# Performance work log

Hardware: AMD Instinct MI355X
Metric: run time of the kernel (lower is better)

The kernel has to match this reference:

```python
import jax, jax.numpy as jnp
import numpy as np

N_NODES = 100000
E = 1600000
IN_C = 128
OUT_C = 128


def setup_inputs() -> dict:
    key = jax.random.key(0)
    k1, k2, k3, k4, k5, k6 = jax.random.split(key, 6)
    x = jax.random.normal(k1, (N_NODES, IN_C), dtype=jnp.float32)
    edge_index = jax.random.randint(k2, (2, E), 0, N_NODES, dtype=jnp.int64)
    s = 1.0 / np.sqrt(IN_C)
    W_src = jax.random.uniform(k3, (OUT_C, IN_C), minval=-s, maxval=s, dtype=jnp.float32)
    b_src = jax.random.uniform(k4, (OUT_C,), minval=-s, maxval=s, dtype=jnp.float32)
    W_dst = jax.random.uniform(k5, (OUT_C, IN_C), minval=-s, maxval=s, dtype=jnp.float32)
    b_dst = jax.random.uniform(k6, (OUT_C,), minval=-s, maxval=s, dtype=jnp.float32)
    return {"x": x, "edge_index": edge_index, "W_src": W_src, "b_src": b_src,
            "W_dst": W_dst, "b_dst": b_dst}


def reference(x, edge_index, W_src, b_src, W_dst, b_dst):
    src, dst = edge_index[0], edge_index[1]
    x_j = x[src]                                             # [E, in]
    agg_sum = jax.ops.segment_sum(x_j, dst, num_segments=x.shape[0])   # [N, in]
    cnt = jax.ops.segment_sum(jnp.ones((src.shape[0],), dtype=x.dtype), dst,
                              num_segments=x.shape[0])       # [N]
    agg_mean = agg_sum / jnp.maximum(cnt, 1.0)[:, None]      # scatter-mean (empty -> 0)
    return agg_mean @ W_src.T + b_src + x @ W_dst.T + b_dst
```

## Files before the change

### kernel.cpp

```cpp
#include <hip/hip_runtime.h>
#include <stdint.h>

typedef __attribute__((ext_vector_type(8))) short short8;
typedef __attribute__((ext_vector_type(4))) float floatx4;
typedef __attribute__((ext_vector_type(4))) int intx4;
typedef __attribute__((ext_vector_type(2))) int intx2;
typedef __attribute__((ext_vector_type(2))) float floatx2;

#define NN 100000
#define NE 1600000
#define NB_SCAN 196
#define HIST_BLKS 6250
#define CONV_BLKS 6250
#define NODES_PER_G 12500
#define CAP 64

#define NBKT 196
#define TILE 4096
#define BIN_BLKS 391
#define CAPB 8704

__device__ __forceinline__ short f2bf(float f) {
  unsigned u = __builtin_bit_cast(unsigned, f);
  u = (u + 0x7fffu + ((u >> 16) & 1u)) >> 16;
  return (short)u;
}
__device__ __forceinline__ float bf2f(unsigned hi16) {
  return __builtin_bit_cast(float, hi16 << 16);
}

#define BK_GC_B 0
#define BK_GBUF_B 4096
#define BK_SLOT_B 14000000
#define BK_ROW_B 21000000
#define BK_DEG_B 21500000
#define BK_XB_B 22000000
#define BK_XQ_B 47600000
#define BK_NEED 60400000ull

#define WS_DEG 0
#define WS_ROW 100000
#define WS_CUR 200000
#define WS_BSUM 300000
#define WS_BOFF 300256
#define WS_SLOT 300512
#define WS_XB_BYTE 7602048


__global__ __launch_bounds__(256) void bin_conv_k(const int* __restrict__ ei,
                                                  int* __restrict__ gcount,
                                                  int2* __restrict__ gbuf,
                                                  const float* __restrict__ x,
                                                  short* __restrict__ xb,
                                                  int* __restrict__ xq) {
  const int blk = blockIdx.x;
  if (blk < BIN_BLKS) {
    __shared__ int ls[TILE], ld[TILE];
    __shared__ int hcnt[NBKT], hbase[NBKT], hcur[NBKT], gposs[NBKT];
    __shared__ int sc[256];
    __shared__ int ntot;
    const int tid = threadIdx.x;
    const int tile = blk * TILE;

    int s_[16], d_[16];
#pragma unroll
    for (int k = 0; k < 16; ++k) {
      const int e = tile + tid + k * 256;
      if (e < NE) {
        s_[k] = ei[e];
        d_[k] = ei[NE + e];
      } else {
        s_[k] = 0; d_[k] = -1;
      }
    }
    if (tid < NBKT) hcnt[tid] = 0;
    __syncthreads();
#pragma unroll
    for (int k = 0; k < 16; ++k)
      if (d_[k] >= 0) atomicAdd(&hcnt[d_[k] >> 9], 1);
    __syncthreads();
    sc[tid] = (tid < NBKT) ? hcnt[tid] : 0;
    __syncthreads();
    for (int off = 1; off < 256; off <<= 1) {
      const int v = (tid >= off) ? sc[tid - off] : 0;
      __syncthreads();
      sc[tid] += v;
      __syncthreads();
    }
    if (tid < NBKT) {
      hbase[tid] = sc[tid] - hcnt[tid];
      gposs[tid] = atomicAdd(&gcount[tid], hcnt[tid]);
      hcur[tid] = 0;
    }
    if (tid == 0) ntot = sc[NBKT - 1];
    __syncthreads();
#pragma unroll
    for (int k = 0; k < 16; ++k) {
      if (d_[k] >= 0) {
        const int b = d_[k] >> 9;
        const int r = hbase[b] + atomicAdd(&hcur[b], 1);
        ls[r] = s_[k];
        ld[r] = d_[k];
      }
    }
    __syncthreads();
    const int nt = ntot;
    for (int i = tid; i < nt; i += 256) {
      const int d = ld[i];
      const int b = d >> 9;
      const int pos = gposs[b] + (i - hbase[b]);
      if (pos < CAPB) {
        int2 e; e.x = ls[i]; e.y = d;
        gbuf[(size_t)b * CAPB + pos] = e;
      }
    }
  } else {
    const int t = (blk - BIN_BLKS) * 256 + threadIdx.x;
    const floatx4* x4 = reinterpret_cast<const floatx4*>(x);
    floatx4 f0 = __builtin_nontemporal_load(&x4[2 * t]);
    floatx4 f1 = __builtin_nontemporal_load(&x4[2 * t + 1]);
    short8 v;
    v[0] = f2bf(f0.x); v[1] = f2bf(f0.y); v[2] = f2bf(f0.z); v[3] = f2bf(f0.w);
    v[4] = f2bf(f1.x); v[5] = f2bf(f1.y); v[6] = f2bf(f1.z); v[7] = f2bf(f1.w);
    reinterpret_cast<short8*>(xb)[t] = v;
    int w0 = __builtin_amdgcn_cvt_pk_fp8_f32(f0.x, f0.y, 0, false);
    w0 = __builtin_amdgcn_cvt_pk_fp8_f32(f0.z, f0.w, w0, true);
    int w1 = __builtin_amdgcn_cvt_pk_fp8_f32(f1.x, f1.y, 0, false);
    w1 = __builtin_amdgcn_cvt_pk_fp8_f32(f1.z, f1.w, w1, true);
    intx2 q; q.x = w0; q.y = w1;
    reinterpret_cast<intx2*>(xq)[t] = q;
  }
}

__global__ __launch_bounds__(512) void bucket_csr_k(const int* __restrict__ gcount,
                                                    const int2* __restrict__ gbuf,
                                                    int* __restrict__ slotg,
                                                    int* __restrict__ rowstg,
                                                    int* __restrict__ degg) {
  __shared__ int cnt[512], sc[512], cur[512];
  __shared__ int lslot[CAPB];
  const int b = blockIdx.x;
  const int tid = threadIdx.x;
  const int nb = min(gcount[b], CAPB);
  const size_t base = (size_t)b * CAPB;

  cnt[tid] = 0;
  __syncthreads();
  for (int i = tid; i < nb; i += 512)
    atomicAdd(&cnt[gbuf[base + i].y & 511], 1);
  __syncthreads();
  sc[tid] = cnt[tid];
  __syncthreads();
  for (int off = 1; off < 512; off <<= 1) {
    const int v = (tid >= off) ? sc[tid - off] : 0;
    __syncthreads();
    sc[tid] += v;
    __syncthreads();
  }
  const int rst = sc[tid] - cnt[tid];
  cur[tid] = rst;
  __syncthreads();
  for (int i = tid; i < nb; i += 512) {
    const int2 e = gbuf[base + i];
    const int p = atomicAdd(&cur[e.y & 511], 1);
    lslot[p] = e.x << 6;
  }
  __syncthreads();
  for (int i = tid; i < nb; i += 512) slotg[base + i] = lslot[i];
  const int n = b * 512 + tid;
  if (n < NN) {
    rowstg[n] = (int)base + rst;
    degg[n] = cnt[tid];
  }
}

__global__ __launch_bounds__(256) void gather_csr_k(const unsigned short* __restrict__ xq,
                                                    const int* __restrict__ rowstg,
                                                    const int* __restrict__ degg,
                                                    const int* __restrict__ slotg,
                                                    float* __restrict__ out) {
  const int lane = threadIdx.x & 63;
  const int w = (blockIdx.x * 256 + threadIdx.x) >> 6;
  if (w >= NN) return;
  const int st = rowstg[w];
  const int dg = degg[w];
  float2 acc = {0.f, 0.f};
  for (int b0 = 0; b0 < dg; b0 += 64) {
    const int nbk = min(64, dg - b0);
    const int idx = (lane < nbk) ? slotg[st + b0 + lane] : 0;
    int i = 0;
    for (; i + 4 <= nbk; i += 4) {
      const int s0 = __shfl(idx, i), s1 = __shfl(idx, i + 1);
      const int s2 = __shfl(idx, i + 2), s3 = __shfl(idx, i + 3);
      const int v0 = xq[s0 + lane];
      const int v1 = xq[s1 + lane];
      const int v2 = xq[s2 + lane];
      const int v3 = xq[s3 + lane];
      floatx2 p0 = __builtin_amdgcn_cvt_pk_f32_fp8(v0, false);
      floatx2 p1 = __builtin_amdgcn_cvt_pk_f32_fp8(v1, false);
      floatx2 p2 = __builtin_amdgcn_cvt_pk_f32_fp8(v2, false);
      floatx2 p3 = __builtin_amdgcn_cvt_pk_f32_fp8(v3, false);
      acc.x += p0.x; acc.y += p0.y;
      acc.x += p1.x; acc.y += p1.y;
      acc.x += p2.x; acc.y += p2.y;
      acc.x += p3.x; acc.y += p3.y;
    }
    for (; i < nbk; ++i) {
      const int s = __shfl(idx, i);
      const int v = xq[s + lane];
      floatx2 p = __builtin_amdgcn_cvt_pk_f32_fp8(v, false);
      acc.x += p.x; acc.y += p.y;
    }
  }
  const float inv = 1.0f / fmaxf((float)dg, 1.0f);
  const unsigned b0w = (unsigned)(unsigned short)f2bf(acc.x * inv);
  const unsigned b1w = (unsigned)(unsigned short)f2bf(acc.y * inv);
  reinterpret_cast<unsigned*>(out + (size_t)w * 128 + 64)[lane] = b0w | (b1w << 16);
}


__global__ __launch_bounds__(256) void hist_conv_k(const int* __restrict__ ei,
                                                   int* __restrict__ deg,
                                                   const float* __restrict__ x,
                                                   short* __restrict__ xb) {
  const int b = blockIdx.x;
  if (b < HIST_BLKS) {
    int e = b * 256 + threadIdx.x;
    if (e < NE) atomicAdd(&deg[ei[NE + e]], 1);
  } else {
    const int t = (b - HIST_BLKS) * 256 + threadIdx.x;
    const float4* x4 = reinterpret_cast<const float4*>(x);
    float4 f0 = x4[2 * t];
    float4 f1 = x4[2 * t + 1];
    short8 v;
    v[0] = f2bf(f0.x); v[1] = f2bf(f0.y); v[2] = f2bf(f0.z); v[3] = f2bf(f0.w);
    v[4] = f2bf(f1.x); v[5] = f2bf(f1.y); v[6] = f2bf(f1.z); v[7] = f2bf(f1.w);
    reinterpret_cast<short8*>(xb)[t] = v;
  }
}

__global__ __launch_bounds__(256) void scan1_k(const int* __restrict__ deg,
                                               int* __restrict__ bsum) {
  __shared__ int s[256];
  const int t = threadIdx.x;
  const int i0 = blockIdx.x * 512 + 2 * t;
  int v = 0;
  if (i0 < NN) v += deg[i0];
  if (i0 + 1 < NN) v += deg[i0 + 1];
  s[t] = v;
  __syncthreads();
  for (int off = 128; off > 0; off >>= 1) {
    if (t < off) s[t] += s[t + off];
    __syncthreads();
  }
  if (t == 0) bsum[blockIdx.x] = s[0];
}

__global__ __launch_bounds__(256) void scan2_k(const int* __restrict__ bsum,
                                               int* __restrict__ boff) {
  __shared__ int s[256];
  const int t = threadIdx.x;
  const int v = (t < NB_SCAN) ? bsum[t] : 0;
  s[t] = v;
  __syncthreads();
  for (int off = 1; off < 256; off <<= 1) {
    int a = (t >= off) ? s[t - off] : 0;
    __syncthreads();
    s[t] += a;
    __syncthreads();
  }
  if (t < NB_SCAN) boff[t] = s[t] - v;
}

__global__ __launch_bounds__(256) void scan3_k(const int* __restrict__ deg,
                                               const int* __restrict__ boff,
                                               int* __restrict__ rowst,
                                               int* __restrict__ cursor) {
  __shared__ int s[256];
  const int t = threadIdx.x;
  const int i0 = blockIdx.x * 512 + 2 * t;
  const int v0 = (i0 < NN) ? deg[i0] : 0;
  const int v1 = (i0 + 1 < NN) ? deg[i0 + 1] : 0;
  const int tsum = v0 + v1;
  s[t] = tsum;
  __syncthreads();
  for (int off = 1; off < 256; off <<= 1) {
    int a = (t >= off) ? s[t - off] : 0;
    __syncthreads();
    s[t] += a;
    __syncthreads();
  }
  const int excl = s[t] - tsum + boff[blockIdx.x];
  if (i0 < NN) { rowst[i0] = excl; cursor[i0] = excl; }
  if (i0 + 1 < NN) { rowst[i0 + 1] = excl + v0; cursor[i0 + 1] = excl + v0; }
}

__global__ __launch_bounds__(256) void fill_k(const int* __restrict__ ei,
                                              int* __restrict__ cursor,
                                              int* __restrict__ slot) {
  const int g = blockIdx.x & 7;
  const int lo = g * NODES_PER_G;
  const int hi = lo + NODES_PER_G;
  const int stride = (gridDim.x >> 3) * 256;
  for (int e = (blockIdx.x >> 3) * 256 + threadIdx.x; e < NE; e += stride) {
    const int d = ei[NE + e];
    if (d >= lo && d < hi) {
      const int p = atomicAdd(&cursor[d], 1);
      slot[p] = ei[e];
    }
  }
}

__global__ __launch_bounds__(256) void gather_bf_k(const short* __restrict__ xb,
                                                   const int* __restrict__ rowst,
                                                   const int* __restrict__ deg,
                                                   const int* __restrict__ slot,
                                                   float* __restrict__ out) {
  const int lane = threadIdx.x & 63;
  const int w = (blockIdx.x * 256 + threadIdx.x) >> 6;
  if (w >= NN) return;
  const int st = rowst[w];
  const int dg = deg[w];
  const unsigned* xu = reinterpret_cast<const unsigned*>(xb);
  float2 acc = {0.f, 0.f};
  for (int b0 = 0; b0 < dg; b0 += 64) {
    const int nb = min(64, dg - b0);
    const int idx = (lane < nb) ? slot[st + b0 + lane] : 0;
    for (int i = 0; i < nb; ++i) {
      const int s = __shfl(idx, i);
      unsigned u = xu[(size_t)s * 64 + lane];
      acc.x += bf2f(u & 0xffffu); acc.y += bf2f(u >> 16);
    }
  }
  const float inv = 1.0f / fmaxf((float)dg, 1.0f);
  const unsigned b0w = (unsigned)(unsigned short)f2bf(acc.x * inv);
  const unsigned b1w = (unsigned)(unsigned short)f2bf(acc.y * inv);
  reinterpret_cast<unsigned*>(out + (size_t)w * 128 + 64)[lane] = b0w | (b1w << 16);
}

__global__ __launch_bounds__(512) void sage_gemm_k(
    const short* __restrict__ xb,
    const float* __restrict__ Wsrc, const float* __restrict__ bsrc,
    const float* __restrict__ Wdst, const float* __restrict__ bdst,
    float* __restrict__ out) {
  __shared__ short Alds[128 * 128];
  __shared__ short Blds[128 * 128];
  const int tid = threadIdx.x;
  const int n0 = blockIdx.x * 128;

  const int wid = tid >> 6;
  const int lane = tid & 63;
  const int r0 = wid * 16;
  const int lrow = lane & 15;
  const int kh = (lane >> 4) * 8;
  const int arow = r0 + lrow;
  const int asw = (arow & 7) << 4;

  floatx4 acc[8];
  floatx4 zero = {0.f, 0.f, 0.f, 0.f};
#pragma unroll
  for (int f = 0; f < 8; ++f) acc[f] = zero;

#pragma unroll
  for (int h = 0; h < 2; ++h) {
    {
      const int j = tid >> 2;
      const int q = tid & 3;
      const float* src = ((h == 0) ? Wsrc : Wdst) + j * 128 + q * 32;
      const int sw = (j & 7) << 4;
      const int base = j * 256 + q * 64;
#pragma unroll
      for (int c = 0; c < 4; ++c) {
        float4 f0 = reinterpret_cast<const float4*>(src)[2 * c];
        float4 f1 = reinterpret_cast<const float4*>(src)[2 * c + 1];
        short8 v;
        v[0] = f2bf(f0.x); v[1] = f2bf(f0.y); v[2] = f2bf(f0.z); v[3] = f2bf(f0.w);
        v[4] = f2bf(f1.x); v[5] = f2bf(f1.y); v[6] = f2bf(f1.z); v[7] = f2bf(f1.w);
        *reinterpret_cast<short8*>(reinterpret_cast<char*>(Blds) + ((base + c * 16) ^ sw)) = v;
      }
    }
    {
      const int r = tid >> 2;
      const int q = tid & 3;
      const int n = n0 + r;
      const int sw = (r & 7) << 4;
      const int base = r * 256 + q * 64;
      if (n < NN) {
        const char* srcb = (h == 0)
            ? (reinterpret_cast<const char*>(out + (size_t)n * 128 + 64) + q * 64)
            : (reinterpret_cast<const char*>(xb + (size_t)n * 128) + q * 64);
#pragma unroll
        for (int c = 0; c < 4; ++c) {
          short8 v = *reinterpret_cast<const short8*>(srcb + c * 16);
          *reinterpret_cast<short8*>(reinterpret_cast<char*>(Alds) + ((base + c * 16) ^ sw)) = v;
        }
      } else {
        short8 z = {};
#pragma unroll
        for (int c = 0; c < 4; ++c)
          *reinterpret_cast<short8*>(reinterpret_cast<char*>(Alds) + ((base + c * 16) ^ sw)) = z;
      }
    }
    __syncthreads();

#pragma unroll
    for (int ks = 0; ks < 4; ++ks) {
      const int kb = (ks * 32 + kh) * 2;
      short8 a = *reinterpret_cast<const short8*>(
          reinterpret_cast<const char*>(Alds) + ((arow * 256 + kb) ^ asw));
#pragma unroll
      for (int f = 0; f < 8; ++f) {
        const int j = f * 16 + lrow;
        short8 b = *reinterpret_cast<const short8*>(
            reinterpret_cast<const char*>(Blds) + ((j * 256 + kb) ^ ((j & 7) << 4)));
        acc[f] = __builtin_amdgcn_mfma_f32_16x16x32_bf16(a, b, acc[f], 0, 0, 0);
      }
    }
    __syncthreads();
  }

  const int crow = r0 + (lane >> 4) * 4;
#pragma unroll
  for (int f = 0; f < 8; ++f) {
    const int j = f * 16 + lrow;
    const float bias = bsrc[j] + bdst[j];
#pragma unroll
    for (int rg = 0; rg < 4; ++rg) {
      const int n = n0 + crow + rg;
      if (n < NN) out[(size_t)n * 128 + j] = acc[f][rg] + bias;
    }
  }
}

extern "C" void kernel_launch(void* const* d_in, const int* in_sizes, int n_in,
                              void* d_out, int out_size, void* d_ws, size_t ws_size,
                              hipStream_t stream) {
  const float* x = (const float*)d_in[0];
  const int* ei = (const int*)d_in[1];
  const float* Wsrc = (const float*)d_in[2];
  const float* bsrc = (const float*)d_in[3];
  const float* Wdst = (const float*)d_in[4];
  const float* bdst = (const float*)d_in[5];
  float* out = (float*)d_out;

  if (ws_size >= BK_NEED) {
    int* gcount = (int*)((char*)d_ws + BK_GC_B);
    int2* gbuf = (int2*)((char*)d_ws + BK_GBUF_B);
    int* slotg = (int*)((char*)d_ws + BK_SLOT_B);
    int* rowstg = (int*)((char*)d_ws + BK_ROW_B);
    int* degg = (int*)((char*)d_ws + BK_DEG_B);
    short* xb = (short*)((char*)d_ws + BK_XB_B);
    int* xq = (int*)((char*)d_ws + BK_XQ_B);
    hipMemsetAsync(gcount, 0, NBKT * sizeof(int), stream);
    bin_conv_k<<<BIN_BLKS + CONV_BLKS, 256, 0, stream>>>(ei, gcount, gbuf, x, xb, xq);
    bucket_csr_k<<<NBKT, 512, 0, stream>>>(gcount, gbuf, slotg, rowstg, degg);
    gather_csr_k<<<(NN * 64 + 255) / 256, 256, 0, stream>>>(
        (const unsigned short*)xq, rowstg, degg, slotg, out);
    sage_gemm_k<<<(NN + 127) / 128, 512, 0, stream>>>(xb, Wsrc, bsrc,
                                                      Wdst, bdst, out);
    return;
  }

  int* ws = (int*)d_ws;
  int* deg = ws + WS_DEG;
  int* rowst = ws + WS_ROW;
  int* cursor = ws + WS_CUR;
  int* bsum = ws + WS_BSUM;
  int* boff = ws + WS_BOFF;
  int* slot = ws + WS_SLOT;
  short* xb = (short*)((char*)d_ws + WS_XB_BYTE);

  hipMemsetAsync(deg, 0, NN * sizeof(int), stream);
  hist_conv_k<<<HIST_BLKS + CONV_BLKS, 256, 0, stream>>>(ei, deg, x, xb);
  scan1_k<<<NB_SCAN, 256, 0, stream>>>(deg, bsum);
  scan2_k<<<1, 256, 0, stream>>>(bsum, boff);
  scan3_k<<<NB_SCAN, 256, 0, stream>>>(deg, boff, rowst, cursor);
  fill_k<<<1024, 256, 0, stream>>>(ei, cursor, slot);
  gather_bf_k<<<(NN * 64 + 255) / 256, 256, 0, stream>>>(xb, rowst, deg, slot, out);
  sage_gemm_k<<<(NN + 127) / 128, 512, 0, stream>>>(xb, Wsrc, bsrc, Wdst, bdst, out);
}
```

Before: 143.4 us.

## Fuse neighbor-mean gather into GEMM kernel and pre-convert weights to bf16

The separate gather kernel, which wrote bf16 mean rows into the output buffer for the GEMM to read back, is merged into a fused kernel. Each 512-thread block gathers the means for its 128 nodes straight into swizzled LDS, runs the W_src MFMA, then loads x rows and the W_dst tile for a second MFMA pass before writing the output with bias. The weights are converted to bf16 once by an extra block in the binning kernel, so the GEMM blocks no longer convert them. This removes a global round trip and a kernel launch. The cost is 64KB of LDS per block, which lowers occupancy, and the latency-bound gather now runs inside a block that holds those resources.

```diff
diff --git a/kernel.cpp b/kernel.cpp
--- a/kernel.cpp
+++ b/kernel.cpp
@@ -36,7 +36,8 @@
 #define BK_DEG_B 21500000
 #define BK_XB_B 22000000
 #define BK_XQ_B 47600000
-#define BK_NEED 60400000ull
+#define BK_WB_B 60400000
+#define BK_NEED 60465536ull
 
 #define WS_DEG 0
 #define WS_ROW 100000
@@ -52,7 +53,10 @@
                                                   int2* __restrict__ gbuf,
                                                   const float* __restrict__ x,
                                                   short* __restrict__ xb,
-                                                  int* __restrict__ xq) {
+                                                  int* __restrict__ xq,
+                                                  const float* __restrict__ Wsrc,
+                                                  const float* __restrict__ Wdst,
+                                                  short* __restrict__ wb) {
   const int blk = blockIdx.x;
   if (blk < BIN_BLKS) {
     __shared__ int ls[TILE], ld[TILE];
@@ -114,7 +118,7 @@
         gbuf[(size_t)b * CAPB + pos] = e;
       }
     }
-  } else {
+  } else if (blk < BIN_BLKS + CONV_BLKS) {
     const int t = (blk - BIN_BLKS) * 256 + threadIdx.x;
     const floatx4* x4 = reinterpret_cast<const floatx4*>(x);
     floatx4 f0 = __builtin_nontemporal_load(&x4[2 * t]);
@@ -129,6 +133,23 @@
     w1 = __builtin_amdgcn_cvt_pk_fp8_f32(f1.z, f1.w, w1, true);
     intx2 q; q.x = w0; q.y = w1;
     reinterpret_cast<intx2*>(xq)[t] = q;
+  } else {
+    const int t = threadIdx.x;
+#pragma unroll
+    for (int m = 0; m < 2; ++m) {
+      const float* W = m ? Wdst : Wsrc;
+      short8* dst = reinterpret_cast<short8*>(wb + m * 16384);
+#pragma unroll
+      for (int c = 0; c < 8; ++c) {
+        const int i8 = t * 8 + c;
+        floatx4 f0 = reinterpret_cast<const floatx4*>(W)[2 * i8];
+        floatx4 f1 = reinterpret_cast<const floatx4*>(W)[2 * i8 + 1];
+        short8 v;
+        v[0] = f2bf(f0.x); v[1] = f2bf(f0.y); v[2] = f2bf(f0.z); v[3] = f2bf(f0.w);
+        v[4] = f2bf(f1.x); v[5] = f2bf(f1.y); v[6] = f2bf(f1.z); v[7] = f2bf(f1.w);
+        dst[i8] = v;
+      }
+    }
   }
 }
 
@@ -174,48 +195,156 @@
   }
 }
 
-__global__ __launch_bounds__(256) void gather_csr_k(const unsigned short* __restrict__ xq,
-                                                    const int* __restrict__ rowstg,
-                                                    const int* __restrict__ degg,
-                                                    const int* __restrict__ slotg,
-                                                    float* __restrict__ out) {
-  const int lane = threadIdx.x & 63;
-  const int w = (blockIdx.x * 256 + threadIdx.x) >> 6;
-  if (w >= NN) return;
-  const int st = rowstg[w];
-  const int dg = degg[w];
-  float2 acc = {0.f, 0.f};
-  for (int b0 = 0; b0 < dg; b0 += 64) {
-    const int nbk = min(64, dg - b0);
-    const int idx = (lane < nbk) ? slotg[st + b0 + lane] : 0;
-    int i = 0;
-    for (; i + 4 <= nbk; i += 4) {
-      const int s0 = __shfl(idx, i), s1 = __shfl(idx, i + 1);
-      const int s2 = __shfl(idx, i + 2), s3 = __shfl(idx, i + 3);
-      const int v0 = xq[s0 + lane];
-      const int v1 = xq[s1 + lane];
-      const int v2 = xq[s2 + lane];
-      const int v3 = xq[s3 + lane];
-      floatx2 p0 = __builtin_amdgcn_cvt_pk_f32_fp8(v0, false);
-      floatx2 p1 = __builtin_amdgcn_cvt_pk_f32_fp8(v1, false);
-      floatx2 p2 = __builtin_amdgcn_cvt_pk_f32_fp8(v2, false);
-      floatx2 p3 = __builtin_amdgcn_cvt_pk_f32_fp8(v3, false);
-      acc.x += p0.x; acc.y += p0.y;
-      acc.x += p1.x; acc.y += p1.y;
-      acc.x += p2.x; acc.y += p2.y;
-      acc.x += p3.x; acc.y += p3.y;
-    }
-    for (; i < nbk; ++i) {
-      const int s = __shfl(idx, i);
-      const int v = xq[s + lane];
-      floatx2 p = __builtin_amdgcn_cvt_pk_f32_fp8(v, false);
-      acc.x += p.x; acc.y += p.y;
-    }
-  }
-  const float inv = 1.0f / fmaxf((float)dg, 1.0f);
-  const unsigned b0w = (unsigned)(unsigned short)f2bf(acc.x * inv);
-  const unsigned b1w = (unsigned)(unsigned short)f2bf(acc.y * inv);
-  reinterpret_cast<unsigned*>(out + (size_t)w * 128 + 64)[lane] = b0w | (b1w << 16);
+__global__ __launch_bounds__(512) void sage_fused_k(
+    const unsigned short* __restrict__ xq, const int* __restrict__ rowstg,
+    const int* __restrict__ degg, const int* __restrict__ slotg,
+    const short* __restrict__ xb, const short* __restrict__ wb,
+    const float* __restrict__ bsrc, const float* __restrict__ bdst,
+    float* __restrict__ out) {
+  __shared__ short Alds[128 * 128];
+  __shared__ short Blds[128 * 128];
+  const int tid = threadIdx.x;
+  const int n0 = blockIdx.x * 128;
+  const int wid = tid >> 6;
+  const int lane = tid & 63;
+  const int r0 = wid * 16;
+  const int lrow = lane & 15;
+  const int kh = (lane >> 4) * 8;
+  const int arow = r0 + lrow;
+  const int asw = (arow & 7) << 4;
+  char* const Ab = reinterpret_cast<char*>(Alds);
+  char* const Bb = reinterpret_cast<char*>(Blds);
+
+  {
+    const int j = tid >> 2;
+    const int q = tid & 3;
+    const short8* src8 = reinterpret_cast<const short8*>(wb + j * 128 + q * 32);
+    const int sw = (j & 7) << 4;
+    const int base = j * 256 + q * 64;
+#pragma unroll
+    for (int c = 0; c < 4; ++c)
+      *reinterpret_cast<short8*>(Bb + ((base + c * 16) ^ sw)) = src8[c];
+  }
+
+  for (int t = 0; t < 16; ++t) {
+    const int row = r0 + t;
+    const int n = n0 + row;
+    unsigned val = 0;
+    if (n < NN) {
+      const int st = rowstg[n];
+      const int dg = degg[n];
+      float2 acc = {0.f, 0.f};
+      for (int b0 = 0; b0 < dg; b0 += 64) {
+        const int nbk = min(64, dg - b0);
+        const int idx = (lane < nbk) ? slotg[st + b0 + lane] : 0;
+        int i = 0;
+        for (; i + 4 <= nbk; i += 4) {
+          const int s0 = __shfl(idx, i), s1 = __shfl(idx, i + 1);
+          const int s2 = __shfl(idx, i + 2), s3 = __shfl(idx, i + 3);
+          const int v0 = xq[s0 + lane];
+          const int v1 = xq[s1 + lane];
+          const int v2 = xq[s2 + lane];
+          const int v3 = xq[s3 + lane];
+          floatx2 p0 = __builtin_amdgcn_cvt_pk_f32_fp8(v0, false);
+          floatx2 p1 = __builtin_amdgcn_cvt_pk_f32_fp8(v1, false);
+          floatx2 p2 = __builtin_amdgcn_cvt_pk_f32_fp8(v2, false);
+          floatx2 p3 = __builtin_amdgcn_cvt_pk_f32_fp8(v3, false);
+          acc.x += p0.x; acc.y += p0.y;
+          acc.x += p1.x; acc.y += p1.y;
+          acc.x += p2.x; acc.y += p2.y;
+          acc.x += p3.x; acc.y += p3.y;
+        }
+        for (; i < nbk; ++i) {
+          const int s = __shfl(idx, i);
+          const int v = xq[s + lane];
+          floatx2 p = __builtin_amdgcn_cvt_pk_f32_fp8(v, false);
+          acc.x += p.x; acc.y += p.y;
+        }
+      }
+      const float inv = 1.0f / fmaxf((float)dg, 1.0f);
+      const unsigned b0w = (unsigned)(unsigned short)f2bf(acc.x * inv);
+      const unsigned b1w = (unsigned)(unsigned short)f2bf(acc.y * inv);
+      val = b0w | (b1w << 16);
+    }
+    *reinterpret_cast<unsigned*>(
+        Ab + ((row * 256 + lane * 4) ^ ((row & 7) << 4))) = val;
+  }
+  __syncthreads();
+
+  floatx4 acc[8];
+  floatx4 zero = {0.f, 0.f, 0.f, 0.f};
+#pragma unroll
+  for (int f = 0; f < 8; ++f) acc[f] = zero;
+
+#pragma unroll
+  for (int ks = 0; ks < 4; ++ks) {
+    const int kb = (ks * 32 + kh) * 2;
+    short8 a = *reinterpret_cast<const short8*>(Ab + ((arow * 256 + kb) ^ asw));
+#pragma unroll
+    for (int f = 0; f < 8; ++f) {
+      const int j = f * 16 + lrow;
+      short8 b = *reinterpret_cast<const short8*>(
+          Bb + ((j * 256 + kb) ^ ((j & 7) << 4)));
+      acc[f] = __builtin_amdgcn_mfma_f32_16x16x32_bf16(a, b, acc[f], 0, 0, 0);
+    }
+  }
+  __syncthreads();
+
+  {
+    const int j = tid >> 2;
+    const int q = tid & 3;
+    const short8* src8 = reinterpret_cast<const short8*>(wb + 16384 + j * 128 + q * 32);
+    const int sw = (j & 7) << 4;
+    const int base = j * 256 + q * 64;
+#pragma unroll
+    for (int c = 0; c < 4; ++c)
+      *reinterpret_cast<short8*>(Bb + ((base + c * 16) ^ sw)) = src8[c];
+  }
+  {
+    const int r = tid >> 2;
+    const int q = tid & 3;
+    const int n = n0 + r;
+    const int sw = (r & 7) << 4;
+    const int base = r * 256 + q * 64;
+    if (n < NN) {
+      const short8* src8 = reinterpret_cast<const short8*>(
+          xb + (size_t)n * 128 + q * 32);
+#pragma unroll
+      for (int c = 0; c < 4; ++c)
+        *reinterpret_cast<short8*>(Ab + ((base + c * 16) ^ sw)) = src8[c];
+    } else {
+      short8 z = {};
+#pragma unroll
+      for (int c = 0; c < 4; ++c)
+        *reinterpret_cast<short8*>(Ab + ((base + c * 16) ^ sw)) = z;
+    }
+  }
+  __syncthreads();
+
+#pragma unroll
+  for (int ks = 0; ks < 4; ++ks) {
+    const int kb = (ks * 32 + kh) * 2;
+    short8 a = *reinterpret_cast<const short8*>(Ab + ((arow * 256 + kb) ^ asw));
+#pragma unroll
+    for (int f = 0; f < 8; ++f) {
+      const int j = f * 16 + lrow;
+      short8 b = *reinterpret_cast<const short8*>(
+          Bb + ((j * 256 + kb) ^ ((j & 7) << 4)));
+      acc[f] = __builtin_amdgcn_mfma_f32_16x16x32_bf16(a, b, acc[f], 0, 0, 0);
+    }
+  }
+
+  const int crow = r0 + (lane >> 4) * 4;
+#pragma unroll
+  for (int f = 0; f < 8; ++f) {
+    const int j = f * 16 + lrow;
+    const float bias = bsrc[j] + bdst[j];
+#pragma unroll
+    for (int rg = 0; rg < 4; ++rg) {
+      const int n = n0 + crow + rg;
+      if (n < NN) out[(size_t)n * 128 + j] = acc[f][rg] + bias;
+    }
+  }
 }
 
 
@@ -451,13 +580,13 @@
     int* degg = (int*)((char*)d_ws + BK_DEG_B);
     short* xb = (short*)((char*)d_ws + BK_XB_B);
     int* xq = (int*)((char*)d_ws + BK_XQ_B);
+    short* wb = (short*)((char*)d_ws + BK_WB_B);
     hipMemsetAsync(gcount, 0, NBKT * sizeof(int), stream);
-    bin_conv_k<<<BIN_BLKS + CONV_BLKS, 256, 0, stream>>>(ei, gcount, gbuf, x, xb, xq);
+    bin_conv_k<<<BIN_BLKS + CONV_BLKS + 1, 256, 0, stream>>>(
+        ei, gcount, gbuf, x, xb, xq, Wsrc, Wdst, wb);
     bucket_csr_k<<<NBKT, 512, 0, stream>>>(gcount, gbuf, slotg, rowstg, degg);
-    gather_csr_k<<<(NN * 64 + 255) / 256, 256, 0, stream>>>(
-        (const unsigned short*)xq, rowstg, degg, slotg, out);
-    sage_gemm_k<<<(NN + 127) / 128, 512, 0, stream>>>(xb, Wsrc, bsrc,
-                                                      Wdst, bdst, out);
+    sage_fused_k<<<(NN + 127) / 128, 512, 0, stream>>>(
+        (const unsigned short*)xq, rowstg, degg, slotg, xb, wb, bsrc, bdst, out);
     return;
   }
 
```

Result: slower. 166.1 us (+15.8%).
